# Performance work log

Measured on AMD Instinct MI355X. Metric: run time of the kernel, lower is better.

Reference implementation:

```python
import jax, jax.numpy as jnp
import numpy as np

N, E = 100000, 1600000
F_IN, HID, C, L = 512, 128, 64, 64
ALPHA, THETA = 0.1, 0.5


def setup_inputs() -> dict:
    key = jax.random.key(0)
    ks = jax.random.split(key, 6)
    x = jax.random.normal(ks[0], (N, F_IN), jnp.float32)
    edge_index = jax.random.randint(ks[1], (2, E), 0, N, jnp.int32)
    W_in = jax.random.normal(ks[2], (F_IN, HID), jnp.float32) * (1.0 / np.sqrt(F_IN))
    b_in = jnp.zeros((HID,), jnp.float32)
    W_convs = jax.random.normal(ks[3], (L, HID, HID), jnp.float32) * (1.0 / np.sqrt(HID))
    W_out = jax.random.normal(ks[4], (HID, C), jnp.float32) * (1.0 / np.sqrt(HID))
    b_out = jnp.zeros((C,), jnp.float32)
    return {"x": x, "edge_index": edge_index, "W_in": W_in, "b_in": b_in,
            "W_convs": W_convs, "W_out": W_out, "b_out": b_out}


def reference(x, edge_index, W_in, b_in, W_convs, W_out, b_out):
    src, dst = edge_index[0], edge_index[1]
    # gcn_norm with self loops: A_hat = D^-1/2 (A + I) D^-1/2
    deg = jax.ops.segment_sum(jnp.ones((E,), x.dtype), dst, num_segments=N) + 1.0
    dinv = jax.lax.rsqrt(deg)
    ew = dinv[src] * dinv[dst]          # [E] off-diagonal weights
    self_w = dinv * dinv                # [N] self-loop weights

    def spmm(h):  # h: [N, HID]
        agg = jax.ops.segment_sum(h[src] * ew[:, None], dst, num_segments=N)
        return agg + self_w[:, None] * h

    # beta_l = log(theta / l + 1), l = 1..L
    betas = jnp.log(THETA / jnp.arange(1, L + 1, dtype=x.dtype) + 1.0)

    x0 = jax.nn.relu(x @ W_in + b_in)   # [N, HID]

    def layer(h, lw):
        W, beta = lw
        p = spmm(h)
        t = (1.0 - ALPHA) * p + ALPHA * x0          # initial residual
        out = (1.0 - beta) * t + beta * (t @ W)     # identity mapping (shared weights)
        return jax.nn.relu(out), None

    z, _ = jax.lax.scan(layer, x0, (W_convs, betas))
    logits = z @ W_out + b_out
    return z, jax.nn.log_softmax(logits, axis=-1)
```

## Files before the change

kernel.cpp:

```cpp
#include <hip/hip_runtime.h>
#include <hip/hip_bf16.h>

#define NN 100000
#define NE 1600000
#define F_IN 512
#define HID 128
#define C_OUT 64
#define L_LAYERS 64
#define SCAN_NB 98

using short8 = __attribute__((ext_vector_type(8))) short;
using f32x4  = __attribute__((ext_vector_type(4))) float;
typedef __attribute__((ext_vector_type(4))) unsigned short ushort4v;

__device__ __forceinline__ short f2bf(float f) {
    __hip_bfloat16 h = __float2bfloat16(f);
    return __builtin_bit_cast(short, h);
}
__device__ __forceinline__ unsigned short f2bfu(float f) {
    __hip_bfloat16 h = __float2bfloat16(f);
    return __builtin_bit_cast(unsigned short, h);
}
__device__ __forceinline__ float bflo(unsigned u) { return __uint_as_float(u << 16); }
__device__ __forceinline__ float bfhi(unsigned u) { return __uint_as_float(u & 0xffff0000u); }
__device__ __forceinline__ float bf2f(unsigned short u) { return __uint_as_float((unsigned)u << 16); }


__global__ void count_deg(const int* __restrict__ dst, int* __restrict__ cnt) {
    int e = blockIdx.x * blockDim.x + threadIdx.x;
    if (e < NE) atomicAdd(&cnt[dst[e]], 1);
}

__global__ void compute_dinv(const int* __restrict__ cnt, float* __restrict__ dinv) {
    int n = blockIdx.x * blockDim.x + threadIdx.x;
    if (n < NN) dinv[n] = rsqrtf((float)cnt[n] + 1.0f);
}

__global__ __launch_bounds__(256) void scan1(const int* __restrict__ cnt,
                                             int* __restrict__ row_ptr,
                                             int* __restrict__ partial) {
    __shared__ int sdata[256];
    int tid = threadIdx.x;
    int base = blockIdx.x * 1024;
    int v[4];
    int idx0 = base + tid * 4;
#pragma unroll
    for (int i = 0; i < 4; ++i) {
        int idx = idx0 + i;
        v[i] = (idx < NN) ? cnt[idx] : 0;
    }
    int s = v[0] + v[1] + v[2] + v[3];
    sdata[tid] = s;
    __syncthreads();
    int x = s;
    for (int off = 1; off < 256; off <<= 1) {
        int y = (tid >= off) ? sdata[tid - off] : 0;
        __syncthreads();
        x += y;
        sdata[tid] = x;
        __syncthreads();
    }
    int run = x - s;
#pragma unroll
    for (int i = 0; i < 4; ++i) {
        int idx = idx0 + i;
        if (idx < NN) row_ptr[idx] = run;
        run += v[i];
    }
    if (tid == 255) partial[blockIdx.x] = x;
}

__global__ __launch_bounds__(128) void scan2(int* __restrict__ partial) {
    __shared__ int sdata[128];
    int tid = threadIdx.x;
    int v = (tid < SCAN_NB) ? partial[tid] : 0;
    sdata[tid] = v;
    __syncthreads();
    int x = v;
    for (int off = 1; off < 128; off <<= 1) {
        int y = (tid >= off) ? sdata[tid - off] : 0;
        __syncthreads();
        x += y;
        sdata[tid] = x;
        __syncthreads();
    }
    if (tid < SCAN_NB) partial[tid] = x - v;
}

__global__ void scan3(int* __restrict__ row_ptr, const int* __restrict__ partial) {
    int idx = blockIdx.x * blockDim.x + threadIdx.x;
    if (idx < NN) row_ptr[idx] += partial[idx >> 10];
    if (idx == 0) row_ptr[NN] = NE;
}

__global__ void scatter_csr(const int* __restrict__ src, const int* __restrict__ dst,
                            const float* __restrict__ dinv, int* __restrict__ fill,
                            int2* __restrict__ edges) {
    int e = blockIdx.x * blockDim.x + threadIdx.x;
    if (e >= NE) return;
    int s = src[e], d = dst[e];
    int pos = atomicAdd(&fill[d], 1);
    edges[pos] = make_int2(s, __float_as_int(dinv[s] * dinv[d]));
}

__global__ __launch_bounds__(256) void prep_wt(const float* __restrict__ Wc,
                                               const float* __restrict__ Win,
                                               __hip_bfloat16* __restrict__ WT,
                                               __hip_bfloat16* __restrict__ WinT) {
    int b = blockIdx.x, tid = threadIdx.x;
    if (b < 64) {
        const float* src = Wc + (size_t)b * HID * HID;
        __hip_bfloat16* dstp = WT + (size_t)b * HID * HID;
        for (int it = 0; it < 64; ++it) {
            int idx = it * 256 + tid;
            int n = idx >> 7, k = idx & 127;
            dstp[idx] = __float2bfloat16(src[k * HID + n]);
        }
    } else {
        int j = b - 64;
        for (int it = 0; it < 16; ++it) {
            int gid = j * 4096 + it * 256 + tid;
            int n = gid >> 9, k = gid & 511;
            WinT[gid] = __float2bfloat16(Win[k * HID + n]);
        }
    }
}

__global__ __launch_bounds__(256) void gemm_x0_mfma(const float* __restrict__ X,
                                                    const __hip_bfloat16* __restrict__ WinT,
                                                    const float* __restrict__ bias,
                                                    __hip_bfloat16* __restrict__ X0b) {
    __shared__ short Xs[128 * 32];
    __shared__ short Ws[128 * 32];
    int tid = threadIdx.x;
    int w = tid >> 6, l = tid & 63, g = l >> 4, r = l & 15;
    int row0 = blockIdx.x * 128;
    f32x4 acc[2][8] = {};

    float4 sx0[2], sx1[2];
    uint4 sw[2];
    auto load_tile = [&](int kt) {
        int k0 = kt * 32;
#pragma unroll
        for (int i = 0; i < 2; ++i) {
            int id = i * 256 + tid;
            int rr = id >> 2, slot = id & 3;
            int grow = row0 + rr;
            sx0[i] = make_float4(0.f, 0.f, 0.f, 0.f); sx1[i] = sx0[i];
            if (grow < NN) {
                sx0[i] = *(const float4*)&X[(size_t)grow * F_IN + k0 + slot * 8];
                sx1[i] = *(const float4*)&X[(size_t)grow * F_IN + k0 + slot * 8 + 4];
            }
            sw[i] = *(const uint4*)&WinT[(size_t)rr * F_IN + k0 + slot * 8];
        }
    };

    load_tile(0);
    for (int kt = 0; kt < 16; ++kt) {
#pragma unroll
        for (int i = 0; i < 2; ++i) {
            int id = i * 256 + tid;
            int rr = id >> 2, slot = id & 3;
            short8 p;
            p[0] = f2bf(sx0[i].x); p[1] = f2bf(sx0[i].y); p[2] = f2bf(sx0[i].z); p[3] = f2bf(sx0[i].w);
            p[4] = f2bf(sx1[i].x); p[5] = f2bf(sx1[i].y); p[6] = f2bf(sx1[i].z); p[7] = f2bf(sx1[i].w);
            *(short8*)&Xs[rr * 32 + (slot ^ ((rr >> 1) & 3)) * 8] = p;
            *(uint4*)&Ws[rr * 32 + (slot ^ ((rr >> 1) & 3)) * 8] = sw[i];
        }
        __syncthreads();
        if (kt < 15) load_tile(kt + 1);
        short8 a[2], bb[8];
#pragma unroll
        for (int m = 0; m < 2; ++m) {
            int row = w * 32 + m * 16 + r;
            a[m] = *(short8*)&Xs[row * 32 + (g ^ ((row >> 1) & 3)) * 8];
        }
#pragma unroll
        for (int n = 0; n < 8; ++n) {
            int row = n * 16 + r;
            bb[n] = *(short8*)&Ws[row * 32 + (g ^ ((row >> 1) & 3)) * 8];
        }
#pragma unroll
        for (int m = 0; m < 2; ++m)
#pragma unroll
            for (int n = 0; n < 8; ++n)
                acc[m][n] = __builtin_amdgcn_mfma_f32_16x16x32_bf16(a[m], bb[n], acc[m][n], 0, 0, 0);
        __syncthreads();
    }
#pragma unroll
    for (int m = 0; m < 2; ++m) {
#pragma unroll
        for (int n = 0; n < 8; ++n) {
            int col = n * 16 + r;
            float bv = bias[col];
#pragma unroll
            for (int q = 0; q < 4; ++q) {
                int row = row0 + w * 32 + m * 16 + g * 4 + q;
                if (row < NN) {
                    float v = fmaxf(acc[m][n][q] + bv, 0.f);
                    X0b[(size_t)row * HID + col] = __float2bfloat16(v);
                }
            }
        }
    }
}

__global__ __launch_bounds__(512, 6) void layer_fused(const unsigned* __restrict__ H2,
                                                      const unsigned* __restrict__ X02,
                                                      const float* __restrict__ dinv,
                                                      const int* __restrict__ row_ptr,
                                                      const int2* __restrict__ edges,
                                                      const __hip_bfloat16* __restrict__ WTl,
                                                      float beta,
                                                      __hip_bfloat16* __restrict__ Hout,
                                                      float* __restrict__ Zf) {
    __shared__ short Ts[64 * 128];
    __shared__ short Ws[128 * 128];
    int tid = threadIdx.x;
    int w = tid >> 6, l = tid & 63, g = l >> 4, r = l & 15;
    int row0 = blockIdx.x * 64;

#pragma unroll
    for (int i = 0; i < 4; ++i) {
        int id = i * 512 + tid;
        int rr = id >> 4, slot = id & 15;
        uint4 wv = *(const uint4*)&WTl[(size_t)id * 8];
        *(uint4*)&Ws[rr * 128 + (slot ^ (rr & 15)) * 8] = wv;
    }

    unsigned* TsU = (unsigned*)Ts;
    for (int i = 0; i < 8; ++i) {
        int rr = w * 8 + i;
        int n = row0 + rr;
        unsigned pk = 0;
        if (n < NN) {
            float dv = dinv[n];
            unsigned hs = H2[((unsigned)n << 6) + l];
            float swt = dv * dv;
            float a0 = swt * bflo(hs), a1 = swt * bfhi(hs);
            int e0 = __builtin_amdgcn_readfirstlane(row_ptr[n]);
            int e1 = __builtin_amdgcn_readfirstlane(row_ptr[n + 1]);
            int e = e0;
            for (; e + 8 <= e1; e += 8) {
                int2 p[8];
#pragma unroll
                for (int u = 0; u < 8; ++u) p[u] = edges[e + u];
                unsigned hv[8];
#pragma unroll
                for (int u = 0; u < 8; ++u)
                    hv[u] = H2[((unsigned)p[u].x << 6) + l];
#pragma unroll
                for (int u = 0; u < 8; ++u) {
                    float ww = __int_as_float(p[u].y);
                    a0 = fmaf(ww, bflo(hv[u]), a0);
                    a1 = fmaf(ww, bfhi(hv[u]), a1);
                }
            }
            for (; e < e1; ++e) {
                int2 p = edges[e];
                unsigned hv = H2[((unsigned)p.x << 6) + l];
                float ww = __int_as_float(p.y);
                a0 = fmaf(ww, bflo(hv), a0);
                a1 = fmaf(ww, bfhi(hv), a1);
            }
            unsigned xv = X02[((unsigned)n << 6) + l];
            a0 = 0.9f * a0 + 0.1f * bflo(xv);
            a1 = 0.9f * a1 + 0.1f * bfhi(xv);
            pk = (unsigned)f2bfu(a0) | ((unsigned)f2bfu(a1) << 16);
        }
        TsU[rr * 64 + ((l >> 2) ^ (rr & 15)) * 4 + (l & 3)] = pk;
    }
    __syncthreads();

    int nb = w & 3, cg = w >> 2;
    f32x4 acc[4] = {};
#pragma unroll
    for (int ks = 0; ks < 4; ++ks) {
        int rrT = nb * 16 + r;
        short8 bT = *(short8*)&Ts[rrT * 128 + ((ks * 4 + g) ^ (rrT & 15)) * 8];
        short8 aW[4];
#pragma unroll
        for (int c = 0; c < 4; ++c) {
            int rrW = (cg * 4 + c) * 16 + r;
            aW[c] = *(short8*)&Ws[rrW * 128 + ((ks * 4 + g) ^ (rrW & 15)) * 8];
        }
#pragma unroll
        for (int c = 0; c < 4; ++c)
            acc[c] = __builtin_amdgcn_mfma_f32_16x16x32_bf16(aW[c], bT, acc[c], 0, 0, 0);
    }

    float omb = 1.0f - beta;
    int node = nb * 16 + r;
    int grow = row0 + node;
    if (grow < NN) {
#pragma unroll
        for (int c = 0; c < 4; ++c) {
            int c0 = (cg * 4 + c) * 16 + g * 4;
            int slotE = c0 >> 3, posE = c0 & 7;
            ushort4v tv = *(ushort4v*)&Ts[node * 128 + (slotE ^ (node & 15)) * 8 + posE];
            float o[4];
#pragma unroll
            for (int q = 0; q < 4; ++q)
                o[q] = fmaxf(omb * bf2f(tv[q]) + beta * acc[c][q], 0.f);
            if (Zf) {
                *(float4*)&Zf[(size_t)grow * HID + c0] = make_float4(o[0], o[1], o[2], o[3]);
            } else {
                ushort4v hv;
#pragma unroll
                for (int q = 0; q < 4; ++q) hv[q] = f2bfu(o[q]);
                *(ushort4v*)&Hout[(size_t)grow * HID + c0] = hv;
            }
        }
    }
}

__global__ __launch_bounds__(64) void final_kernel(const float* __restrict__ Z,
                                                   const float* __restrict__ Wout,
                                                   const float* __restrict__ bout,
                                                   float* __restrict__ lo) {
    int n = blockIdx.x;
    int c = threadIdx.x;
    float logit = bout[c];
    for (int k = 0; k < HID; ++k) {
        logit = fmaf(Z[(size_t)n * HID + k], Wout[k * C_OUT + c], logit);
    }
    float m = logit;
#pragma unroll
    for (int off = 32; off; off >>= 1) m = fmaxf(m, __shfl_xor(m, off));
    float ex = __expf(logit - m);
    float ssum = ex;
#pragma unroll
    for (int off = 32; off; off >>= 1) ssum += __shfl_xor(ssum, off);
    lo[(size_t)n * C_OUT + c] = logit - m - logf(ssum);
}

extern "C" void kernel_launch(void* const* d_in, const int* in_sizes, int n_in,
                              void* d_out, int out_size, void* d_ws, size_t ws_size,
                              hipStream_t stream) {
    const float* x = (const float*)d_in[0];
    const int* ei = (const int*)d_in[1];
    const int* src = ei;
    const int* dst = ei + NE;
    const float* W_in = (const float*)d_in[2];
    const float* b_in = (const float*)d_in[3];
    const float* W_convs = (const float*)d_in[4];
    const float* W_out = (const float*)d_in[5];
    const float* b_out = (const float*)d_in[6];
    float* out = (float*)d_out;

    char* ws = (char*)d_ws;
    float* dinv = (float*)ws;              ws += (size_t)NN * 4;
    int* row_ptr = (int*)ws;               ws += (size_t)(NN + 4) * 4;
    int* fill = (int*)ws;                  ws += (size_t)NN * 4;
    int* partial = (int*)ws;               ws += (size_t)128 * 4;
    int2* edges = (int2*)ws;               ws += (size_t)NE * 8;
    __hip_bfloat16* WT = (__hip_bfloat16*)ws;   ws += (size_t)L_LAYERS * HID * HID * 2;
    __hip_bfloat16* WinT = (__hip_bfloat16*)ws; ws += (size_t)F_IN * HID * 2;
    __hip_bfloat16* x0b = (__hip_bfloat16*)ws;  ws += (size_t)NN * HID * 2;
    __hip_bfloat16* HbA = (__hip_bfloat16*)ws;  ws += (size_t)NN * HID * 2;
    __hip_bfloat16* HbB = (__hip_bfloat16*)ws;  ws += (size_t)NN * HID * 2;

    hipMemsetAsync(fill, 0, (size_t)NN * 4, stream);
    count_deg<<<(NE + 255) / 256, 256, 0, stream>>>(dst, fill);
    compute_dinv<<<(NN + 255) / 256, 256, 0, stream>>>(fill, dinv);
    scan1<<<SCAN_NB, 256, 0, stream>>>(fill, row_ptr, partial);
    scan2<<<1, 128, 0, stream>>>(partial);
    scan3<<<(NN + 255) / 256, 256, 0, stream>>>(row_ptr, partial);
    hipMemcpyAsync(fill, row_ptr, (size_t)NN * 4, hipMemcpyDeviceToDevice, stream);
    scatter_csr<<<(NE + 255) / 256, 256, 0, stream>>>(src, dst, dinv, fill, edges);
    prep_wt<<<80, 256, 0, stream>>>(W_convs, W_in, WT, WinT);

    int gemm_blocks = (NN + 127) / 128;
    gemm_x0_mfma<<<gemm_blocks, 256, 0, stream>>>(x, WinT, b_in, x0b);

    int layer_blocks = (NN + 63) / 64;
    float* zf = out;
    for (int l = 0; l < L_LAYERS; ++l) {
        const __hip_bfloat16* h_in = (l == 0) ? x0b : ((l & 1) ? HbA : HbB);
        __hip_bfloat16* h_out = (l & 1) ? HbB : HbA;
        float beta = logf(0.5f / (float)(l + 1) + 1.0f);
        bool last = (l == L_LAYERS - 1);
        layer_fused<<<layer_blocks, 512, 0, stream>>>(
            (const unsigned*)h_in, (const unsigned*)x0b, dinv, row_ptr, edges,
            WT + (size_t)l * HID * HID, beta,
            h_out, last ? zf : (float*)nullptr);
    }

    final_kernel<<<NN, 64, 0, stream>>>(zf, W_out, b_out, out + (size_t)NN * HID);
}
```

Measured before the change: 7.830 ms.

## Interleave two-node neighbor gathers, double-buffer x0 GEMM LDS, and stage coalesced output

```diff
diff --git a/kernel.cpp b/kernel.cpp
--- a/kernel.cpp
+++ b/kernel.cpp
@@ -90,7 +90,7 @@
 __global__ void scan3(int* __restrict__ row_ptr, const int* __restrict__ partial) {
     int idx = blockIdx.x * blockDim.x + threadIdx.x;
     if (idx < NN) row_ptr[idx] += partial[idx >> 10];
-    if (idx == 0) row_ptr[NN] = NE;
+    else if (idx <= NN + 64) row_ptr[idx] = NE;
 }
 
 __global__ void scatter_csr(const int* __restrict__ src, const int* __restrict__ dst,
@@ -130,8 +130,7 @@
                                                     const __hip_bfloat16* __restrict__ WinT,
                                                     const float* __restrict__ bias,
                                                     __hip_bfloat16* __restrict__ X0b) {
-    __shared__ short Xs[128 * 32];
-    __shared__ short Ws[128 * 32];
+    __shared__ short SMEM[128 * 128];
     int tid = threadIdx.x;
     int w = tid >> 6, l = tid & 63, g = l >> 4, r = l & 15;
     int row0 = blockIdx.x * 128;
@@ -139,7 +138,7 @@
 
     float4 sx0[2], sx1[2];
     uint4 sw[2];
-    auto load_tile = [&](int kt) {
+    auto load_regs = [&](int kt) {
         int k0 = kt * 32;
 #pragma unroll
         for (int i = 0; i < 2; ++i) {
@@ -155,8 +154,10 @@
         }
     };
 
-    load_tile(0);
+    load_regs(0);
     for (int kt = 0; kt < 16; ++kt) {
+        short* Xs = SMEM + (kt & 1) * 4096;
+        short* Wsh = SMEM + 8192 + (kt & 1) * 4096;
 #pragma unroll
         for (int i = 0; i < 2; ++i) {
             int id = i * 256 + tid;
@@ -165,10 +166,10 @@
             p[0] = f2bf(sx0[i].x); p[1] = f2bf(sx0[i].y); p[2] = f2bf(sx0[i].z); p[3] = f2bf(sx0[i].w);
             p[4] = f2bf(sx1[i].x); p[5] = f2bf(sx1[i].y); p[6] = f2bf(sx1[i].z); p[7] = f2bf(sx1[i].w);
             *(short8*)&Xs[rr * 32 + (slot ^ ((rr >> 1) & 3)) * 8] = p;
-            *(uint4*)&Ws[rr * 32 + (slot ^ ((rr >> 1) & 3)) * 8] = sw[i];
+            *(uint4*)&Wsh[rr * 32 + (slot ^ ((rr >> 1) & 3)) * 8] = sw[i];
         }
         __syncthreads();
-        if (kt < 15) load_tile(kt + 1);
+        if (kt < 15) load_regs(kt + 1);
         short8 a[2], bb[8];
 #pragma unroll
         for (int m = 0; m < 2; ++m) {
@@ -178,15 +179,15 @@
 #pragma unroll
         for (int n = 0; n < 8; ++n) {
             int row = n * 16 + r;
-            bb[n] = *(short8*)&Ws[row * 32 + (g ^ ((row >> 1) & 3)) * 8];
+            bb[n] = *(short8*)&Wsh[row * 32 + (g ^ ((row >> 1) & 3)) * 8];
         }
 #pragma unroll
         for (int m = 0; m < 2; ++m)
 #pragma unroll
             for (int n = 0; n < 8; ++n)
                 acc[m][n] = __builtin_amdgcn_mfma_f32_16x16x32_bf16(a[m], bb[n], acc[m][n], 0, 0, 0);
-        __syncthreads();
-    }
+    }
+    __syncthreads();
 #pragma unroll
     for (int m = 0; m < 2; ++m) {
 #pragma unroll
@@ -195,13 +196,21 @@
             float bv = bias[col];
 #pragma unroll
             for (int q = 0; q < 4; ++q) {
-                int row = row0 + w * 32 + m * 16 + g * 4 + q;
-                if (row < NN) {
-                    float v = fmaxf(acc[m][n][q] + bv, 0.f);
-                    X0b[(size_t)row * HID + col] = __float2bfloat16(v);
-                }
-            }
-        }
+                int row = w * 32 + m * 16 + g * 4 + q;
+                float v = fmaxf(acc[m][n][q] + bv, 0.f);
+                SMEM[row * 128 + ((col >> 3) ^ (row & 15)) * 8 + (col & 7)] = f2bf(v);
+            }
+        }
+    }
+    __syncthreads();
+#pragma unroll
+    for (int i = 0; i < 8; ++i) {
+        int id = i * 256 + tid;
+        int rr = id >> 4, c8 = id & 15;
+        int grow = row0 + rr;
+        if (grow < NN)
+            *(uint4*)&X0b[(size_t)grow * HID + c8 * 8] =
+                *(uint4*)&SMEM[rr * 128 + ((c8 ^ (rr & 15)) * 8)];
     }
 }
 
@@ -229,46 +238,62 @@
     }
 
     unsigned* TsU = (unsigned*)Ts;
-    for (int i = 0; i < 8; ++i) {
-        int rr = w * 8 + i;
-        int n = row0 + rr;
-        unsigned pk = 0;
-        if (n < NN) {
-            float dv = dinv[n];
-            unsigned hs = H2[((unsigned)n << 6) + l];
-            float swt = dv * dv;
-            float a0 = swt * bflo(hs), a1 = swt * bfhi(hs);
-            int e0 = __builtin_amdgcn_readfirstlane(row_ptr[n]);
-            int e1 = __builtin_amdgcn_readfirstlane(row_ptr[n + 1]);
-            int e = e0;
-            for (; e + 8 <= e1; e += 8) {
-                int2 p[8];
-#pragma unroll
-                for (int u = 0; u < 8; ++u) p[u] = edges[e + u];
-                unsigned hv[8];
-#pragma unroll
-                for (int u = 0; u < 8; ++u)
-                    hv[u] = H2[((unsigned)p[u].x << 6) + l];
-#pragma unroll
-                for (int u = 0; u < 8; ++u) {
-                    float ww = __int_as_float(p[u].y);
-                    a0 = fmaf(ww, bflo(hv[u]), a0);
-                    a1 = fmaf(ww, bfhi(hv[u]), a1);
-                }
-            }
-            for (; e < e1; ++e) {
-                int2 p = edges[e];
-                unsigned hv = H2[((unsigned)p.x << 6) + l];
-                float ww = __int_as_float(p.y);
-                a0 = fmaf(ww, bflo(hv), a0);
-                a1 = fmaf(ww, bfhi(hv), a1);
-            }
-            unsigned xv = X02[((unsigned)n << 6) + l];
-            a0 = 0.9f * a0 + 0.1f * bflo(xv);
-            a1 = 0.9f * a1 + 0.1f * bfhi(xv);
-            pk = (unsigned)f2bfu(a0) | ((unsigned)f2bfu(a1) << 16);
-        }
-        TsU[rr * 64 + ((l >> 2) ^ (rr & 15)) * 4 + (l & 3)] = pk;
+    int nb0 = row0 + w * 8;
+    int ep[9];
+#pragma unroll
+    for (int k = 0; k < 9; ++k) ep[k] = __builtin_amdgcn_readfirstlane(row_ptr[nb0 + k]);
+
+#pragma unroll
+    for (int j = 0; j < 4; ++j) {
+        int rrA = w * 8 + 2 * j, rrB = rrA + 1;
+        int nA = row0 + rrA, nB = nA + 1;
+        bool vA = nA < NN, vB = nB < NN;
+        unsigned hsA = vA ? H2[((unsigned)nA << 6) + l] : 0u;
+        unsigned hsB = vB ? H2[((unsigned)nB << 6) + l] : 0u;
+        unsigned xvA = vA ? X02[((unsigned)nA << 6) + l] : 0u;
+        unsigned xvB = vB ? X02[((unsigned)nB << 6) + l] : 0u;
+        float dvA = vA ? dinv[nA] : 0.f, dvB = vB ? dinv[nB] : 0.f;
+        float a0A = dvA * dvA * bflo(hsA), a1A = dvA * dvA * bfhi(hsA);
+        float a0B = dvB * dvB * bflo(hsB), a1B = dvB * dvB * bfhi(hsB);
+        int eA = ep[2 * j], e1A = ep[2 * j + 1];
+        int eB = e1A, e1B = ep[2 * j + 2];
+        while (eA < e1A || eB < e1B) {
+            int cA = e1A - eA; cA = cA > 8 ? 8 : (cA < 0 ? 0 : cA);
+            int cB = e1B - eB; cB = cB > 8 ? 8 : (cB < 0 ? 0 : cB);
+            int sA[8], sB[8];
+            float wA[8], wB[8];
+#pragma unroll
+            for (int u = 0; u < 8; ++u) {
+                int2 t = edges[eA + u];
+                sA[u] = (u < cA) ? t.x : 0;
+                wA[u] = (u < cA) ? __int_as_float(t.y) : 0.f;
+            }
+#pragma unroll
+            for (int u = 0; u < 8; ++u) {
+                int2 t = edges[eB + u];
+                sB[u] = (u < cB) ? t.x : 0;
+                wB[u] = (u < cB) ? __int_as_float(t.y) : 0.f;
+            }
+            unsigned hvA[8], hvB[8];
+#pragma unroll
+            for (int u = 0; u < 8; ++u) hvA[u] = H2[((unsigned)sA[u] << 6) + l];
+#pragma unroll
+            for (int u = 0; u < 8; ++u) hvB[u] = H2[((unsigned)sB[u] << 6) + l];
+#pragma unroll
+            for (int u = 0; u < 8; ++u) {
+                a0A = fmaf(wA[u], bflo(hvA[u]), a0A);
+                a1A = fmaf(wA[u], bfhi(hvA[u]), a1A);
+                a0B = fmaf(wB[u], bflo(hvB[u]), a0B);
+                a1B = fmaf(wB[u], bfhi(hvB[u]), a1B);
+            }
+            eA += cA; eB += cB;
+        }
+        a0A = 0.9f * a0A + 0.1f * bflo(xvA);  a1A = 0.9f * a1A + 0.1f * bfhi(xvA);
+        a0B = 0.9f * a0B + 0.1f * bflo(xvB);  a1B = 0.9f * a1B + 0.1f * bfhi(xvB);
+        unsigned pkA = (unsigned)f2bfu(a0A) | ((unsigned)f2bfu(a1A) << 16);
+        unsigned pkB = (unsigned)f2bfu(a0B) | ((unsigned)f2bfu(a1B) << 16);
+        TsU[rrA * 64 + ((l >> 2) ^ (rrA & 15)) * 4 + (l & 3)] = pkA;
+        TsU[rrB * 64 + ((l >> 2) ^ (rrB & 15)) * 4 + (l & 3)] = pkB;
     }
     __syncthreads();
 
@@ -350,10 +375,10 @@
 
     char* ws = (char*)d_ws;
     float* dinv = (float*)ws;              ws += (size_t)NN * 4;
-    int* row_ptr = (int*)ws;               ws += (size_t)(NN + 4) * 4;
+    int* row_ptr = (int*)ws;               ws += (size_t)(NN + 72) * 4;
     int* fill = (int*)ws;                  ws += (size_t)NN * 4;
     int* partial = (int*)ws;               ws += (size_t)128 * 4;
-    int2* edges = (int2*)ws;               ws += (size_t)NE * 8;
+    int2* edges = (int2*)ws;               ws += (size_t)(NE + 8) * 8;
     __hip_bfloat16* WT = (__hip_bfloat16*)ws;   ws += (size_t)L_LAYERS * HID * HID * 2;
     __hip_bfloat16* WinT = (__hip_bfloat16*)ws; ws += (size_t)F_IN * HID * 2;
     __hip_bfloat16* x0b = (__hip_bfloat16*)ws;  ws += (size_t)NN * HID * 2;
```

After: 6.369 ms. -18.7%, faster.
